# Performance work log

Hardware: AMD Instinct MI355X
Metric: run time of the kernel (lower is better)

The kernel has to match this reference:

```python
import jax, jax.numpy as jnp
import numpy as np

NUM_NEIGHBORS = (10, 25)  # FLAGS.num_neighbors = '10_25'
MAX_DEGREE = 64
L = 2  # num encoder layers


def _sample(nodes, neighbors_out, neighbors_in, key):
    """Multi-hop uniform neighbor sampling (shuffle columns + slice, as in TF code)."""
    samples = [nodes]
    support = 1
    supports = [1]
    for k in range(L):
        t = L - 1 - k
        n = NUM_NEIGHBORS[t]
        support *= 2 * n
        supports.append(support)
        key, k1, k2 = jax.random.split(key, 3)
        # tf.transpose(tf.random.shuffle(tf.transpose(x))) shuffles neighbor slots
        # with ONE permutation shared across all rows, then slices first n.
        cols_out = jax.random.permutation(k1, MAX_DEGREE)[:n]
        cols_in = jax.random.permutation(k2, MAX_DEGREE)[:n]
        nout = neighbors_out[samples[k]][:, cols_out]  # [prev, n]
        nin = neighbors_in[samples[k]][:, cols_in]     # [prev, n]
        samples.append(jnp.concatenate([nout, nin], axis=1).reshape(-1))
    return samples, supports


def _gc(self_v, nei_out, nei_in, W):
    # GraphConvolution: mean-aggregate out/in neighbors, concat with self, linear, sigmoid.
    agg = jnp.concatenate([self_v, nei_out.mean(axis=1), nei_in.mean(axis=1)], axis=-1)
    return jax.nn.sigmoid(agg @ W)


def _aggregate(inputs, supports, layer, W, B):
    h_hop = []
    for hop in range(L - layer):
        n = NUM_NEIGHBORS[L - hop - 1]
        nei = inputs[hop + 1].reshape(B * supports[hop], 2 * n, -1)
        self_v = inputs[hop].reshape(B * supports[hop], -1)
        h_hop.append(_gc(self_v, nei[:, :n], nei[:, n:], W))
    return h_hop


def _forward(nodes1, nodes2, neighbors_out, neighbors_in, features,
             W_in, W_mean, W_std, W_pi, W_ag, W_ad, Wd_mean, Wd_std, Wd_pi):
    B = nodes1.shape[0]
    key = jax.random.key(42)
    k1, k2 = jax.random.split(key)
    s1, sup1 = _sample(nodes1, neighbors_out, neighbors_in, k1)
    s2, sup2 = _sample(nodes2, neighbors_out, neighbors_in, k2)
    in1 = [features[s] for s in s1]  # hop-wise gathered features
    in2 = [features[s] for s in s2]
    # layer 0: shared input GC
    h1 = _aggregate(in1, sup1, 0, W_in, B)
    h2 = _aggregate(in2, sup2, 0, W_in, B)
    # layer 1: parameter heads (mean/std/pi/alpha)
    h_mean1 = _aggregate(h1, sup1, 1, W_mean, B)[0]
    h_mean2 = _aggregate(h2, sup2, 1, W_mean, B)[0]
    h_std1 = _aggregate(h1, sup1, 1, W_std, B)[0]
    h_std2 = _aggregate(h2, sup2, 1, W_std, B)[0]
    h_pi1 = _aggregate(h1, sup1, 1, W_pi, B)[0]
    h_pi2 = _aggregate(h2, sup2, 1, W_pi, B)[0]
    # final fully-connected projections (act = identity)
    z_mean1 = h_mean1 @ Wd_mean
    z_mean2 = h_mean2 @ Wd_mean
    z_std1 = h_std1 @ Wd_std
    z_std2 = h_std2 @ Wd_std
    pi_logit1 = h_pi1 @ Wd_pi
    pi_logit2 = h_pi2 @ Wd_pi
    return jnp.stack([z_mean1, z_std1, pi_logit1, z_mean2, z_std2, pi_logit2])


def setup_inputs() -> dict:
    key = jax.random.key(0)
    ks = jax.random.split(key, 16)
    N, F, B = 200000, 128, 256
    E, D = 128, 64
    inp = {
        'nodes1': jax.random.randint(ks[0], (B,), 0, N, dtype=jnp.int32),
        'nodes2': jax.random.randint(ks[1], (B,), 0, N, dtype=jnp.int32),
        'neighbors_out': jax.random.randint(ks[2], (N, MAX_DEGREE), 0, N, dtype=jnp.int32),
        'neighbors_in': jax.random.randint(ks[3], (N, MAX_DEGREE), 0, N, dtype=jnp.int32),
        'features': jax.random.normal(ks[4], (N, F), dtype=jnp.float32),
        'W_in': jax.random.normal(ks[5], (3 * F, E), dtype=jnp.float32) * 0.05,
        'W_mean': jax.random.normal(ks[6], (3 * E, E), dtype=jnp.float32) * 0.05,
        'W_std': jax.random.normal(ks[7], (3 * E, E), dtype=jnp.float32) * 0.05,
        'W_pi': jax.random.normal(ks[8], (3 * E, E), dtype=jnp.float32) * 0.05,
        'W_ag': jax.random.normal(ks[9], (3 * E, E), dtype=jnp.float32) * 0.05,
        'W_ad': jax.random.normal(ks[10], (3 * E, E), dtype=jnp.float32) * 0.05,
        'Wd_mean': jax.random.normal(ks[11], (E, D), dtype=jnp.float32) * 0.05,
        'Wd_std': jax.random.normal(ks[12], (E, D), dtype=jnp.float32) * 0.05,
        'Wd_pi': jax.random.normal(ks[13], (E, D), dtype=jnp.float32) * 0.05,
    }
    return inp


def reference(nodes1, nodes2, neighbors_out, neighbors_in, features,
              W_in, W_mean, W_std, W_pi, W_ag, W_ad, Wd_mean, Wd_std, Wd_pi):
    return _forward(nodes1, nodes2, neighbors_out, neighbors_in, features,
                    W_in, W_mean, W_std, W_pi, W_ag, W_ad, Wd_mean, Wd_std, Wd_pi)
```

## Files before the change

kernel.cpp:

```cpp
#include <hip/hip_runtime.h>
#include <stdint.h>
#include <math.h>

#define FDIM 128
#define KDIM 384
#define NROWS 26112

struct Cols { int o25[25]; int i25[25]; int o10[10]; int i10[10]; };
struct ColsBoth { Cols c[2]; };

static inline uint32_t rotl32(uint32_t x, uint32_t r){ return (x<<r)|(x>>(32u-r)); }

static void tf2x32(uint32_t k0, uint32_t k1, uint32_t c0, uint32_t c1,
                   uint32_t& o0, uint32_t& o1){
  const uint32_t ra[4] = {13u,15u,26u,6u};
  const uint32_t rb[4] = {17u,29u,16u,24u};
  uint32_t ks2 = k0 ^ k1 ^ 0x1BD11BDAu;
  uint32_t x0 = c0 + k0, x1 = c1 + k1;
  for(int i=0;i<4;i++){ x0 += x1; x1 = rotl32(x1, ra[i]); x1 ^= x0; }
  x0 += k1; x1 += ks2 + 1u;
  for(int i=0;i<4;i++){ x0 += x1; x1 = rotl32(x1, rb[i]); x1 ^= x0; }
  x0 += ks2; x1 += k0 + 2u;
  for(int i=0;i<4;i++){ x0 += x1; x1 = rotl32(x1, ra[i]); x1 ^= x0; }
  x0 += k0; x1 += k1 + 3u;
  for(int i=0;i<4;i++){ x0 += x1; x1 = rotl32(x1, rb[i]); x1 ^= x0; }
  x0 += k1; x1 += ks2 + 4u;
  for(int i=0;i<4;i++){ x0 += x1; x1 = rotl32(x1, ra[i]); x1 ^= x0; }
  x0 += ks2; x1 += k0 + 5u;
  o0 = x0; o1 = x1;
}

static void jax_split_child(uint32_t ka, uint32_t kb, uint32_t i,
                            uint32_t& oa, uint32_t& ob){
  tf2x32(ka, kb, 0u, i, oa, ob);
}

static uint32_t jax_bits32(uint32_t ka, uint32_t kb, uint32_t i){
  uint32_t a,b; tf2x32(ka, kb, 0u, i, a, b);
  return a ^ b;
}

static void jax_perm64(uint32_t ka, uint32_t kb, int* perm){
  uint32_t sa, sb; jax_split_child(ka, kb, 1u, sa, sb);
  uint32_t b[64]; int v[64];
  for(int i=0;i<64;i++){ b[i]=jax_bits32(sa, sb, (uint32_t)i); v[i]=i; }
  for(int i=1;i<64;i++){
    uint32_t bb=b[i]; int vv=v[i]; int j=i-1;
    while(j>=0 && b[j]>bb){ b[j+1]=b[j]; v[j+1]=v[j]; j--; }
    b[j+1]=bb; v[j+1]=vv;
  }
  for(int i=0;i<64;i++) perm[i]=v[i];
}

static void compute_cols(ColsBoth& cb){
  uint32_t k1a,k1b,k2a,k2b;
  jax_split_child(0u, 42u, 0u, k1a, k1b);
  jax_split_child(0u, 42u, 1u, k2a, k2b);
  for(int side=0; side<2; side++){
    uint32_t ka = side ? k2a : k1a;
    uint32_t kb = side ? k2b : k1b;
    uint32_t nka,nkb, c1a,c1b, c2a,c2b;
    jax_split_child(ka,kb,0u,nka,nkb);
    jax_split_child(ka,kb,1u,c1a,c1b);
    jax_split_child(ka,kb,2u,c2a,c2b);
    int p[64];
    jax_perm64(c1a,c1b,p); for(int i=0;i<25;i++) cb.c[side].o25[i]=p[i];
    jax_perm64(c2a,c2b,p); for(int i=0;i<25;i++) cb.c[side].i25[i]=p[i];
    uint32_t d1a,d1b,d2a,d2b;
    jax_split_child(nka,nkb,1u,d1a,d1b);
    jax_split_child(nka,nkb,2u,d2a,d2b);
    jax_perm64(d1a,d1b,p); for(int i=0;i<10;i++) cb.c[side].o10[i]=p[i];
    jax_perm64(d2a,d2b,p); for(int i=0;i<10;i++) cb.c[side].i10[i]=p[i];
  }
}

__device__ __forceinline__ float getc(const float4& v, int i){
  return (i==0)?v.x:(i==1)?v.y:(i==2)?v.z:v.w;
}
__device__ __forceinline__ float sigf(float x){ return 1.0f/(1.0f+expf(-x)); }
__device__ __forceinline__ void add4(float4& s, const float4& v){
  s.x+=v.x; s.y+=v.y; s.z+=v.z; s.w+=v.w;
}


__global__ __launch_bounds__(256) void sample1_kernel(
    const int* __restrict__ nodes1, const int* __restrict__ nodes2,
    const int* __restrict__ nout, const int* __restrict__ nin,
    int* __restrict__ s_hop1, ColsBoth cb){
  int idx = blockIdx.x*blockDim.x + threadIdx.x;
  if(idx >= 2*256*50) return;
  int side = idx / (256*50);
  int rem  = idx % (256*50);
  int b = rem / 50, j = rem % 50;
  int node = (side ? nodes2 : nodes1)[b];
  const Cols& c = cb.c[side];
  int nbr = (j < 25) ? nout[(long)node*64 + c.o25[j]]
                     : nin [(long)node*64 + c.i25[j-25]];
  s_hop1[idx] = nbr;
}

__global__ __launch_bounds__(256) void gather_kernel(
    const float* __restrict__ feat,
    const int* __restrict__ nodes1, const int* __restrict__ nodes2,
    const int* __restrict__ s_hop1,
    const int* __restrict__ nout, const int* __restrict__ nin,
    float* __restrict__ agg, int base_row, ColsBoth cb)
{
  int t = threadIdx.x;
  int row_local = blockIdx.x*8 + (t>>5);
  int lane = t & 31;
  int c0 = lane*4;
  int row = base_row + row_local;

  float4 selfv, so, si;

  if(row < 512){
    int side = row >> 8, b = row & 255;
    int node = (side ? nodes2 : nodes1)[b];
    selfv = *(const float4*)(feat + (long)node*FDIM + c0);
    const int* nb = s_hop1 + row*50;
    float4 acc = make_float4(0,0,0,0);
    #pragma unroll
    for(int jj=0; jj<25; jj+=5){
      int id[5]; float4 v[5];
      #pragma unroll
      for(int i=0;i<5;i++) id[i] = nb[jj+i];
      #pragma unroll
      for(int i=0;i<5;i++) v[i] = *(const float4*)(feat + (long)id[i]*FDIM + c0);
      #pragma unroll
      for(int i=0;i<5;i++) add4(acc, v[i]);
    }
    so = make_float4(acc.x/25.f, acc.y/25.f, acc.z/25.f, acc.w/25.f);
    acc = make_float4(0,0,0,0);
    #pragma unroll
    for(int jj=25; jj<50; jj+=5){
      int id[5]; float4 v[5];
      #pragma unroll
      for(int i=0;i<5;i++) id[i] = nb[jj+i];
      #pragma unroll
      for(int i=0;i<5;i++) v[i] = *(const float4*)(feat + (long)id[i]*FDIM + c0);
      #pragma unroll
      for(int i=0;i<5;i++) add4(acc, v[i]);
    }
    si = make_float4(acc.x/25.f, acc.y/25.f, acc.z/25.f, acc.w/25.f);
  } else {
    int hrow = row - 512;
    int side = (hrow >= 12800) ? 1 : 0;
    int node = s_hop1[hrow];
    const Cols& c = cb.c[side];
    const long nb = (long)node*64;
    int oid[10], iid[10];
    #pragma unroll
    for(int j=0;j<10;j++) oid[j] = nout[nb + c.o10[j]];
    #pragma unroll
    for(int j=0;j<10;j++) iid[j] = nin[nb + c.i10[j]];
    selfv = *(const float4*)(feat + (long)node*FDIM + c0);
    float4 v[10];
    #pragma unroll
    for(int j=0;j<10;j++) v[j] = *(const float4*)(feat + (long)oid[j]*FDIM + c0);
    float4 acc = make_float4(0,0,0,0);
    #pragma unroll
    for(int j=0;j<10;j++) add4(acc, v[j]);
    so = make_float4(acc.x*0.1f, acc.y*0.1f, acc.z*0.1f, acc.w*0.1f);
    #pragma unroll
    for(int j=0;j<10;j++) v[j] = *(const float4*)(feat + (long)iid[j]*FDIM + c0);
    acc = make_float4(0,0,0,0);
    #pragma unroll
    for(int j=0;j<10;j++) add4(acc, v[j]);
    si = make_float4(acc.x*0.1f, acc.y*0.1f, acc.z*0.1f, acc.w*0.1f);
  }

  float* ar = agg + (long)row_local*KDIM;
  *(float4*)(ar + c0)       = selfv;
  *(float4*)(ar + 128 + c0) = so;
  *(float4*)(ar + 256 + c0) = si;
}

__global__ __launch_bounds__(256) void gemm_sig_kernel(
    const float* __restrict__ A, const float* __restrict__ W,
    float* __restrict__ out)
{
  __shared__ float Wbuf[96*128];
  int t = threadIdx.x, lane = t&15, rg = t>>4;
  int r0 = blockIdx.x*64 + rg*4;
  int c0 = lane*8;
  float acc[4][8];
  #pragma unroll
  for(int r=0;r<4;r++)
    #pragma unroll
    for(int i=0;i<8;i++) acc[r][i]=0.f;

  for(int kc=0; kc<4; kc++){
    __syncthreads();
    const float4* ws = (const float4*)(W + kc*96*128);
    float4* wd = (float4*)Wbuf;
    #pragma unroll
    for(int i=0;i<12;i++) wd[i*256+t] = ws[i*256+t];
    __syncthreads();
    const float* Ab = A + (long)r0*KDIM + kc*96;
    #pragma unroll 2
    for(int k4=0;k4<96;k4+=4){
      float4 a0 = *(const float4*)(Ab + 0*KDIM + k4);
      float4 a1 = *(const float4*)(Ab + 1*KDIM + k4);
      float4 a2 = *(const float4*)(Ab + 2*KDIM + k4);
      float4 a3 = *(const float4*)(Ab + 3*KDIM + k4);
      #pragma unroll
      for(int kk=0;kk<4;kk++){
        float av0=getc(a0,kk), av1=getc(a1,kk), av2=getc(a2,kk), av3=getc(a3,kk);
        const float* wr = Wbuf + (k4+kk)*128 + c0;
        float4 w0 = *(const float4*)wr;
        float4 w1 = *(const float4*)(wr+4);
        acc[0][0]+=av0*w0.x; acc[0][1]+=av0*w0.y; acc[0][2]+=av0*w0.z; acc[0][3]+=av0*w0.w;
        acc[0][4]+=av0*w1.x; acc[0][5]+=av0*w1.y; acc[0][6]+=av0*w1.z; acc[0][7]+=av0*w1.w;
        acc[1][0]+=av1*w0.x; acc[1][1]+=av1*w0.y; acc[1][2]+=av1*w0.z; acc[1][3]+=av1*w0.w;
        acc[1][4]+=av1*w1.x; acc[1][5]+=av1*w1.y; acc[1][6]+=av1*w1.z; acc[1][7]+=av1*w1.w;
        acc[2][0]+=av2*w0.x; acc[2][1]+=av2*w0.y; acc[2][2]+=av2*w0.z; acc[2][3]+=av2*w0.w;
        acc[2][4]+=av2*w1.x; acc[2][5]+=av2*w1.y; acc[2][6]+=av2*w1.z; acc[2][7]+=av2*w1.w;
        acc[3][0]+=av3*w0.x; acc[3][1]+=av3*w0.y; acc[3][2]+=av3*w0.z; acc[3][3]+=av3*w0.w;
        acc[3][4]+=av3*w1.x; acc[3][5]+=av3*w1.y; acc[3][6]+=av3*w1.z; acc[3][7]+=av3*w1.w;
      }
    }
  }
  #pragma unroll
  for(int r=0;r<4;r++){
    float4 o0, o1;
    o0.x=sigf(acc[r][0]); o0.y=sigf(acc[r][1]); o0.z=sigf(acc[r][2]); o0.w=sigf(acc[r][3]);
    o1.x=sigf(acc[r][4]); o1.y=sigf(acc[r][5]); o1.z=sigf(acc[r][6]); o1.w=sigf(acc[r][7]);
    float* op = out + (long)(r0+r)*FDIM + c0;
    *(float4*)op = o0; *(float4*)(op+4) = o1;
  }
}

__global__ __launch_bounds__(256) void agg1_kernel(
    const float* __restrict__ h0, const float* __restrict__ h1,
    float* __restrict__ agg2)
{
  int row = blockIdx.x;
  int t = threadIdx.x;
  int ch = t & 127;
  int half = t >> 7;
  const float* base = h1 + (long)row*50*FDIM + half*25*FDIM + ch;
  float s = 0.f;
  #pragma unroll
  for(int j=0;j<25;j++) s += base[j*FDIM];
  agg2[(long)row*KDIM + 128 + half*128 + ch] = s * (1.0f/25.0f);
  if(half == 0) agg2[(long)row*KDIM + ch] = h0[(long)row*FDIM + ch];
}

__global__ __launch_bounds__(256) void head_kernel(
    const float* __restrict__ agg2,
    const float* __restrict__ Wm, const float* __restrict__ Ws, const float* __restrict__ Wp,
    const float* __restrict__ Dm, const float* __restrict__ Ds, const float* __restrict__ Dp,
    float* __restrict__ out)
{
  __shared__ float Wbuf[96*128];
  __shared__ float hb[64*133];
  int t = threadIdx.x, lane = t&15, rg = t>>4;
  int head = blockIdx.x >> 3, tile = blockIdx.x & 7;
  int r0t = tile*64;
  int r0 = r0t + rg*4;
  int c0 = lane*8;
  const float* W = (head==0) ? Wm : (head==1) ? Ws : Wp;
  const float* D = (head==0) ? Dm : (head==1) ? Ds : Dp;

  float acc[4][8];
  #pragma unroll
  for(int r=0;r<4;r++)
    #pragma unroll
    for(int i=0;i<8;i++) acc[r][i]=0.f;

  for(int kc=0; kc<4; kc++){
    __syncthreads();
    const float4* ws = (const float4*)(W + kc*96*128);
    float4* wd = (float4*)Wbuf;
    #pragma unroll
    for(int i=0;i<12;i++) wd[i*256+t] = ws[i*256+t];
    __syncthreads();
    const float* Ab = agg2 + (long)r0*KDIM + kc*96;
    #pragma unroll 2
    for(int k4=0;k4<96;k4+=4){
      float4 a0 = *(const float4*)(Ab + 0*KDIM + k4);
      float4 a1 = *(const float4*)(Ab + 1*KDIM + k4);
      float4 a2 = *(const float4*)(Ab + 2*KDIM + k4);
      float4 a3 = *(const float4*)(Ab + 3*KDIM + k4);
      #pragma unroll
      for(int kk=0;kk<4;kk++){
        float av0=getc(a0,kk), av1=getc(a1,kk), av2=getc(a2,kk), av3=getc(a3,kk);
        const float* wr = Wbuf + (k4+kk)*128 + c0;
        float4 w0 = *(const float4*)wr;
        float4 w1 = *(const float4*)(wr+4);
        acc[0][0]+=av0*w0.x; acc[0][1]+=av0*w0.y; acc[0][2]+=av0*w0.z; acc[0][3]+=av0*w0.w;
        acc[0][4]+=av0*w1.x; acc[0][5]+=av0*w1.y; acc[0][6]+=av0*w1.z; acc[0][7]+=av0*w1.w;
        acc[1][0]+=av1*w0.x; acc[1][1]+=av1*w0.y; acc[1][2]+=av1*w0.z; acc[1][3]+=av1*w0.w;
        acc[1][4]+=av1*w1.x; acc[1][5]+=av1*w1.y; acc[1][6]+=av1*w1.z; acc[1][7]+=av1*w1.w;
        acc[2][0]+=av2*w0.x; acc[2][1]+=av2*w0.y; acc[2][2]+=av2*w0.z; acc[2][3]+=av2*w0.w;
        acc[2][4]+=av2*w1.x; acc[2][5]+=av2*w1.y; acc[2][6]+=av2*w1.z; acc[2][7]+=av2*w1.w;
        acc[3][0]+=av3*w0.x; acc[3][1]+=av3*w0.y; acc[3][2]+=av3*w0.z; acc[3][3]+=av3*w0.w;
        acc[3][4]+=av3*w1.x; acc[3][5]+=av3*w1.y; acc[3][6]+=av3*w1.z; acc[3][7]+=av3*w1.w;
      }
    }
  }
  #pragma unroll
  for(int r=0;r<4;r++){
    float* hp = hb + (rg*4+r)*133 + c0;
    #pragma unroll
    for(int i=0;i<8;i++) hp[i] = sigf(acc[r][i]);
  }
  __syncthreads();
  {
    const float4* ds = (const float4*)D;
    float4* dd = (float4*)Wbuf;
    #pragma unroll
    for(int i=0;i<8;i++) dd[i*256+t] = ds[i*256+t];
  }
  __syncthreads();
  {
    int cd = lane*4;
    float a2[4][4];
    #pragma unroll
    for(int r=0;r<4;r++)
      #pragma unroll
      for(int i=0;i<4;i++) a2[r][i]=0.f;
    #pragma unroll 4
    for(int k=0;k<FDIM;k++){
      float4 d = *(const float4*)(Wbuf + k*64 + cd);
      #pragma unroll
      for(int r=0;r<4;r++){
        float hv = hb[(rg*4+r)*133 + k];
        a2[r][0]+=hv*d.x; a2[r][1]+=hv*d.y; a2[r][2]+=hv*d.z; a2[r][3]+=hv*d.w;
      }
    }
    #pragma unroll
    for(int r=0;r<4;r++){
      int row = r0 + r;
      int side = row >> 8, b = row & 255;
      float* op = out + ((long)(side*3+head)*256 + b)*64 + cd;
      *(float4*)op = make_float4(a2[r][0],a2[r][1],a2[r][2],a2[r][3]);
    }
  }
}

extern "C" void kernel_launch(void* const* d_in, const int* in_sizes, int n_in,
                              void* d_out, int out_size, void* d_ws, size_t ws_size,
                              hipStream_t stream) {
  const int*   nodes1  = (const int*)d_in[0];
  const int*   nodes2  = (const int*)d_in[1];
  const int*   nout    = (const int*)d_in[2];
  const int*   nin     = (const int*)d_in[3];
  const float* feat    = (const float*)d_in[4];
  const float* W_in    = (const float*)d_in[5];
  const float* W_mean  = (const float*)d_in[6];
  const float* W_std   = (const float*)d_in[7];
  const float* W_pi    = (const float*)d_in[8];
  const float* Wd_mean = (const float*)d_in[11];
  const float* Wd_std  = (const float*)d_in[12];
  const float* Wd_pi   = (const float*)d_in[13];
  float* out = (float*)d_out;

  int*   s_hop1 = (int*)d_ws;
  float* h      = (float*)(s_hop1 + 25600);
  float* agg2   = h + (size_t)NROWS*FDIM;
  float* aggC   = agg2 + 512*KDIM;

  size_t fixedB = 25600*4 + (size_t)NROWS*FDIM*4 + 512*KDIM*4;
  const int ncOpt[5] = {1,2,4,8,24};
  int nc = 24;
  for(int i=0;i<5;i++){
    size_t need = fixedB + ((size_t)NROWS/ncOpt[i])*KDIM*4;
    if(need <= ws_size){ nc = ncOpt[i]; break; }
  }
  int chunkRows = NROWS / nc;

  ColsBoth cb;
  compute_cols(cb);

  sample1_kernel<<<(2*256*50 + 255)/256, 256, 0, stream>>>(nodes1, nodes2, nout, nin, s_hop1, cb);
  for(int c=0;c<nc;c++){
    int base = c*chunkRows;
    gather_kernel<<<chunkRows/8, 256, 0, stream>>>(feat, nodes1, nodes2, s_hop1,
                                                   nout, nin, aggC, base, cb);
    gemm_sig_kernel<<<chunkRows/64, 256, 0, stream>>>(aggC, W_in, h + (size_t)base*FDIM);
  }
  agg1_kernel<<<512, 256, 0, stream>>>(h, h + 512*FDIM, agg2);
  head_kernel<<<24, 256, 0, stream>>>(agg2, W_mean, W_std, W_pi, Wd_mean, Wd_std, Wd_pi, out);
}
```

Baseline: 333.6 us.

## Fuse hop-1 aggregation into head kernel, enlarge GEMM row tile, batch gathers

Merges the agg1 and head kernels into one agghead kernel. It builds the 384-wide aggregated rows in shared memory and runs the head GEMM and the decoder straight from global weights over 96 blocks of 16 rows each, which removes the agg2 round trip and one launch. The main layer-0 GEMM now computes 8 rows per thread (128-row tiles), which raises register use but halves the number of shared-memory weight reads per FMA. The gather kernel now issues all 20 hop-1 neighbor loads before reducing, and the chunk-count options change so they divide evenly into 128-row tiles.

Measured after the change: 355.7 us. 6.6% more time.

```diff
diff --git a/kernel.cpp b/kernel.cpp
--- a/kernel.cpp
+++ b/kernel.cpp
@@ -155,18 +155,18 @@
     #pragma unroll
     for(int j=0;j<10;j++) iid[j] = nin[nb + c.i10[j]];
     selfv = *(const float4*)(feat + (long)node*FDIM + c0);
-    float4 v[10];
-    #pragma unroll
-    for(int j=0;j<10;j++) v[j] = *(const float4*)(feat + (long)oid[j]*FDIM + c0);
+    float4 v[20];
+    #pragma unroll
+    for(int j=0;j<10;j++) v[j]    = *(const float4*)(feat + (long)oid[j]*FDIM + c0);
+    #pragma unroll
+    for(int j=0;j<10;j++) v[10+j] = *(const float4*)(feat + (long)iid[j]*FDIM + c0);
     float4 acc = make_float4(0,0,0,0);
     #pragma unroll
     for(int j=0;j<10;j++) add4(acc, v[j]);
     so = make_float4(acc.x*0.1f, acc.y*0.1f, acc.z*0.1f, acc.w*0.1f);
-    #pragma unroll
-    for(int j=0;j<10;j++) v[j] = *(const float4*)(feat + (long)iid[j]*FDIM + c0);
     acc = make_float4(0,0,0,0);
     #pragma unroll
-    for(int j=0;j<10;j++) add4(acc, v[j]);
+    for(int j=0;j<10;j++) add4(acc, v[10+j]);
     si = make_float4(acc.x*0.1f, acc.y*0.1f, acc.z*0.1f, acc.w*0.1f);
   }
 
@@ -182,11 +182,11 @@
 {
   __shared__ float Wbuf[96*128];
   int t = threadIdx.x, lane = t&15, rg = t>>4;
-  int r0 = blockIdx.x*64 + rg*4;
+  int r0 = blockIdx.x*128 + rg*8;
   int c0 = lane*8;
-  float acc[4][8];
+  float acc[8][8];
   #pragma unroll
-  for(int r=0;r<4;r++)
+  for(int r=0;r<8;r++)
     #pragma unroll
     for(int i=0;i<8;i++) acc[r][i]=0.f;
 
@@ -198,31 +198,26 @@
     for(int i=0;i<12;i++) wd[i*256+t] = ws[i*256+t];
     __syncthreads();
     const float* Ab = A + (long)r0*KDIM + kc*96;
-    #pragma unroll 2
     for(int k4=0;k4<96;k4+=4){
-      float4 a0 = *(const float4*)(Ab + 0*KDIM + k4);
-      float4 a1 = *(const float4*)(Ab + 1*KDIM + k4);
-      float4 a2 = *(const float4*)(Ab + 2*KDIM + k4);
-      float4 a3 = *(const float4*)(Ab + 3*KDIM + k4);
+      float4 a[8];
+      #pragma unroll
+      for(int r=0;r<8;r++) a[r] = *(const float4*)(Ab + r*KDIM + k4);
       #pragma unroll
       for(int kk=0;kk<4;kk++){
-        float av0=getc(a0,kk), av1=getc(a1,kk), av2=getc(a2,kk), av3=getc(a3,kk);
         const float* wr = Wbuf + (k4+kk)*128 + c0;
         float4 w0 = *(const float4*)wr;
         float4 w1 = *(const float4*)(wr+4);
-        acc[0][0]+=av0*w0.x; acc[0][1]+=av0*w0.y; acc[0][2]+=av0*w0.z; acc[0][3]+=av0*w0.w;
-        acc[0][4]+=av0*w1.x; acc[0][5]+=av0*w1.y; acc[0][6]+=av0*w1.z; acc[0][7]+=av0*w1.w;
-        acc[1][0]+=av1*w0.x; acc[1][1]+=av1*w0.y; acc[1][2]+=av1*w0.z; acc[1][3]+=av1*w0.w;
-        acc[1][4]+=av1*w1.x; acc[1][5]+=av1*w1.y; acc[1][6]+=av1*w1.z; acc[1][7]+=av1*w1.w;
-        acc[2][0]+=av2*w0.x; acc[2][1]+=av2*w0.y; acc[2][2]+=av2*w0.z; acc[2][3]+=av2*w0.w;
-        acc[2][4]+=av2*w1.x; acc[2][5]+=av2*w1.y; acc[2][6]+=av2*w1.z; acc[2][7]+=av2*w1.w;
-        acc[3][0]+=av3*w0.x; acc[3][1]+=av3*w0.y; acc[3][2]+=av3*w0.z; acc[3][3]+=av3*w0.w;
-        acc[3][4]+=av3*w1.x; acc[3][5]+=av3*w1.y; acc[3][6]+=av3*w1.z; acc[3][7]+=av3*w1.w;
+        #pragma unroll
+        for(int r=0;r<8;r++){
+          float av = getc(a[r],kk);
+          acc[r][0]+=av*w0.x; acc[r][1]+=av*w0.y; acc[r][2]+=av*w0.z; acc[r][3]+=av*w0.w;
+          acc[r][4]+=av*w1.x; acc[r][5]+=av*w1.y; acc[r][6]+=av*w1.z; acc[r][7]+=av*w1.w;
+        }
       }
     }
   }
   #pragma unroll
-  for(int r=0;r<4;r++){
+  for(int r=0;r<8;r++){
     float4 o0, o1;
     o0.x=sigf(acc[r][0]); o0.y=sigf(acc[r][1]); o0.z=sigf(acc[r][2]); o0.w=sigf(acc[r][3]);
     o1.x=sigf(acc[r][4]); o1.y=sigf(acc[r][5]); o1.z=sigf(acc[r][6]); o1.w=sigf(acc[r][7]);
@@ -231,112 +226,86 @@
   }
 }
 
-__global__ __launch_bounds__(256) void agg1_kernel(
-    const float* __restrict__ h0, const float* __restrict__ h1,
-    float* __restrict__ agg2)
-{
-  int row = blockIdx.x;
-  int t = threadIdx.x;
-  int ch = t & 127;
-  int half = t >> 7;
-  const float* base = h1 + (long)row*50*FDIM + half*25*FDIM + ch;
-  float s = 0.f;
-  #pragma unroll
-  for(int j=0;j<25;j++) s += base[j*FDIM];
-  agg2[(long)row*KDIM + 128 + half*128 + ch] = s * (1.0f/25.0f);
-  if(half == 0) agg2[(long)row*KDIM + ch] = h0[(long)row*FDIM + ch];
-}
-
-__global__ __launch_bounds__(256) void head_kernel(
-    const float* __restrict__ agg2,
+__global__ __launch_bounds__(256) void agghead_kernel(
+    const float* __restrict__ h,
     const float* __restrict__ Wm, const float* __restrict__ Ws, const float* __restrict__ Wp,
     const float* __restrict__ Dm, const float* __restrict__ Ds, const float* __restrict__ Dp,
     float* __restrict__ out)
 {
-  __shared__ float Wbuf[96*128];
-  __shared__ float hb[64*133];
+  __shared__ float agg[16][388];
+  __shared__ float hb[16][132];
+  int head = blockIdx.x >> 5, tile = blockIdx.x & 31;
   int t = threadIdx.x, lane = t&15, rg = t>>4;
-  int head = blockIdx.x >> 3, tile = blockIdx.x & 7;
-  int r0t = tile*64;
-  int r0 = r0t + rg*4;
+  int row = tile*16 + rg;
   int c0 = lane*8;
   const float* W = (head==0) ? Wm : (head==1) ? Ws : Wp;
   const float* D = (head==0) ? Dm : (head==1) ? Ds : Dp;
 
-  float acc[4][8];
-  #pragma unroll
-  for(int r=0;r<4;r++)
-    #pragma unroll
-    for(int i=0;i<8;i++) acc[r][i]=0.f;
-
-  for(int kc=0; kc<4; kc++){
-    __syncthreads();
-    const float4* ws = (const float4*)(W + kc*96*128);
-    float4* wd = (float4*)Wbuf;
-    #pragma unroll
-    for(int i=0;i<12;i++) wd[i*256+t] = ws[i*256+t];
-    __syncthreads();
-    const float* Ab = agg2 + (long)r0*KDIM + kc*96;
-    #pragma unroll 2
-    for(int k4=0;k4<96;k4+=4){
-      float4 a0 = *(const float4*)(Ab + 0*KDIM + k4);
-      float4 a1 = *(const float4*)(Ab + 1*KDIM + k4);
-      float4 a2 = *(const float4*)(Ab + 2*KDIM + k4);
-      float4 a3 = *(const float4*)(Ab + 3*KDIM + k4);
-      #pragma unroll
-      for(int kk=0;kk<4;kk++){
-        float av0=getc(a0,kk), av1=getc(a1,kk), av2=getc(a2,kk), av3=getc(a3,kk);
-        const float* wr = Wbuf + (k4+kk)*128 + c0;
-        float4 w0 = *(const float4*)wr;
-        float4 w1 = *(const float4*)(wr+4);
-        acc[0][0]+=av0*w0.x; acc[0][1]+=av0*w0.y; acc[0][2]+=av0*w0.z; acc[0][3]+=av0*w0.w;
-        acc[0][4]+=av0*w1.x; acc[0][5]+=av0*w1.y; acc[0][6]+=av0*w1.z; acc[0][7]+=av0*w1.w;
-        acc[1][0]+=av1*w0.x; acc[1][1]+=av1*w0.y; acc[1][2]+=av1*w0.z; acc[1][3]+=av1*w0.w;
-        acc[1][4]+=av1*w1.x; acc[1][5]+=av1*w1.y; acc[1][6]+=av1*w1.z; acc[1][7]+=av1*w1.w;
-        acc[2][0]+=av2*w0.x; acc[2][1]+=av2*w0.y; acc[2][2]+=av2*w0.z; acc[2][3]+=av2*w0.w;
-        acc[2][4]+=av2*w1.x; acc[2][5]+=av2*w1.y; acc[2][6]+=av2*w1.z; acc[2][7]+=av2*w1.w;
-        acc[3][0]+=av3*w0.x; acc[3][1]+=av3*w0.y; acc[3][2]+=av3*w0.z; acc[3][3]+=av3*w0.w;
-        acc[3][4]+=av3*w1.x; acc[3][5]+=av3*w1.y; acc[3][6]+=av3*w1.z; acc[3][7]+=av3*w1.w;
+  {
+    const float* sp = h + (long)row*FDIM + c0;
+    *(float4*)&agg[rg][c0]   = *(const float4*)sp;
+    *(float4*)&agg[rg][c0+4] = *(const float4*)(sp+4);
+    const float* base = h + (long)(512 + row*50)*FDIM + c0;
+    float4 s0 = make_float4(0,0,0,0), s1 = make_float4(0,0,0,0);
+    #pragma unroll
+    for(int jj=0;jj<25;jj+=5){
+      float4 v0[5], v1[5];
+      #pragma unroll
+      for(int i=0;i<5;i++){
+        const float* fp = base + (long)(jj+i)*FDIM;
+        v0[i] = *(const float4*)fp; v1[i] = *(const float4*)(fp+4);
       }
-    }
-  }
-  #pragma unroll
-  for(int r=0;r<4;r++){
-    float* hp = hb + (rg*4+r)*133 + c0;
-    #pragma unroll
-    for(int i=0;i<8;i++) hp[i] = sigf(acc[r][i]);
+      #pragma unroll
+      for(int i=0;i<5;i++){ add4(s0, v0[i]); add4(s1, v1[i]); }
+    }
+    const float inv = 1.0f/25.0f;
+    *(float4*)&agg[rg][128+c0]   = make_float4(s0.x*inv,s0.y*inv,s0.z*inv,s0.w*inv);
+    *(float4*)&agg[rg][128+c0+4] = make_float4(s1.x*inv,s1.y*inv,s1.z*inv,s1.w*inv);
+    s0 = make_float4(0,0,0,0); s1 = make_float4(0,0,0,0);
+    #pragma unroll
+    for(int jj=25;jj<50;jj+=5){
+      float4 v0[5], v1[5];
+      #pragma unroll
+      for(int i=0;i<5;i++){
+        const float* fp = base + (long)(jj+i)*FDIM;
+        v0[i] = *(const float4*)fp; v1[i] = *(const float4*)(fp+4);
+      }
+      #pragma unroll
+      for(int i=0;i<5;i++){ add4(s0, v0[i]); add4(s1, v1[i]); }
+    }
+    *(float4*)&agg[rg][256+c0]   = make_float4(s0.x*inv,s0.y*inv,s0.z*inv,s0.w*inv);
+    *(float4*)&agg[rg][256+c0+4] = make_float4(s1.x*inv,s1.y*inv,s1.z*inv,s1.w*inv);
   }
   __syncthreads();
+
   {
-    const float4* ds = (const float4*)D;
-    float4* dd = (float4*)Wbuf;
-    #pragma unroll
-    for(int i=0;i<8;i++) dd[i*256+t] = ds[i*256+t];
+    float acc[8] = {0,0,0,0,0,0,0,0};
+    #pragma unroll 4
+    for(int k=0;k<KDIM;k++){
+      float a = agg[rg][k];
+      const float* wr = W + (long)k*FDIM + c0;
+      float4 w0 = *(const float4*)wr; float4 w1 = *(const float4*)(wr+4);
+      acc[0]+=a*w0.x; acc[1]+=a*w0.y; acc[2]+=a*w0.z; acc[3]+=a*w0.w;
+      acc[4]+=a*w1.x; acc[5]+=a*w1.y; acc[6]+=a*w1.z; acc[7]+=a*w1.w;
+    }
+    #pragma unroll
+    for(int i=0;i<8;i++) hb[rg][c0+i] = sigf(acc[i]);
   }
   __syncthreads();
+
   {
     int cd = lane*4;
-    float a2[4][4];
-    #pragma unroll
-    for(int r=0;r<4;r++)
-      #pragma unroll
-      for(int i=0;i<4;i++) a2[r][i]=0.f;
+    float a0=0,a1=0,a2=0,a3=0;
     #pragma unroll 4
     for(int k=0;k<FDIM;k++){
-      float4 d = *(const float4*)(Wbuf + k*64 + cd);
-      #pragma unroll
-      for(int r=0;r<4;r++){
-        float hv = hb[(rg*4+r)*133 + k];
-        a2[r][0]+=hv*d.x; a2[r][1]+=hv*d.y; a2[r][2]+=hv*d.z; a2[r][3]+=hv*d.w;
-      }
-    }
-    #pragma unroll
-    for(int r=0;r<4;r++){
-      int row = r0 + r;
-      int side = row >> 8, b = row & 255;
-      float* op = out + ((long)(side*3+head)*256 + b)*64 + cd;
-      *(float4*)op = make_float4(a2[r][0],a2[r][1],a2[r][2],a2[r][3]);
-    }
+      float hv = hb[rg][k];
+      const float* dr = D + (long)k*64 + cd;
+      float4 d = *(const float4*)dr;
+      a0 += hv*d.x; a1 += hv*d.y; a2 += hv*d.z; a3 += hv*d.w;
+    }
+    int side = row >> 8, b = row & 255;
+    float* op = out + ((long)(side*3+head)*256 + b)*64 + cd;
+    *(float4*)op = make_float4(a0,a1,a2,a3);
   }
 }
 
@@ -359,12 +328,11 @@
 
   int*   s_hop1 = (int*)d_ws;
   float* h      = (float*)(s_hop1 + 25600);
-  float* agg2   = h + (size_t)NROWS*FDIM;
-  float* aggC   = agg2 + 512*KDIM;
-
-  size_t fixedB = 25600*4 + (size_t)NROWS*FDIM*4 + 512*KDIM*4;
-  const int ncOpt[5] = {1,2,4,8,24};
-  int nc = 24;
+  float* aggC   = h + (size_t)NROWS*FDIM;
+
+  size_t fixedB = 25600*4 + (size_t)NROWS*FDIM*4;
+  const int ncOpt[5] = {1,2,4,12,51};
+  int nc = 51;
   for(int i=0;i<5;i++){
     size_t need = fixedB + ((size_t)NROWS/ncOpt[i])*KDIM*4;
     if(need <= ws_size){ nc = ncOpt[i]; break; }
@@ -379,8 +347,7 @@
     int base = c*chunkRows;
     gather_kernel<<<chunkRows/8, 256, 0, stream>>>(feat, nodes1, nodes2, s_hop1,
                                                    nout, nin, aggC, base, cb);
-    gemm_sig_kernel<<<chunkRows/64, 256, 0, stream>>>(aggC, W_in, h + (size_t)base*FDIM);
-  }
-  agg1_kernel<<<512, 256, 0, stream>>>(h, h + 512*FDIM, agg2);
-  head_kernel<<<24, 256, 0, stream>>>(agg2, W_mean, W_std, W_pi, Wd_mean, Wd_std, Wd_pi, out);
-}
+    gemm_sig_kernel<<<chunkRows/128, 256, 0, stream>>>(aggC, W_in, h + (size_t)base*FDIM);
+  }
+  agghead_kernel<<<96, 256, 0, stream>>>(h, W_mean, W_std, W_pi, Wd_mean, Wd_std, Wd_pi, out);
+}
```

## Spread head kernel across many small blocks, batch hop-1 gather loads

Applied to the files above, without the earlier changes.

The head kernel now gives each block 4 rows, so 384 blocks run instead of 24. Weights are read directly from global memory or cache instead of being staged and tiled in shared memory, which trades register tiling for parallelism across the GPU. The gather kernel issues all 20 neighbour loads before reducing, for more memory-level parallelism. The fallback chunk counts change so chunkRows stays a multiple of 64.

Result: no change. 331.1 us (-0.8%).

```diff
diff --git a/kernel.cpp b/kernel.cpp
--- a/kernel.cpp
+++ b/kernel.cpp
@@ -155,18 +155,18 @@
     #pragma unroll
     for(int j=0;j<10;j++) iid[j] = nin[nb + c.i10[j]];
     selfv = *(const float4*)(feat + (long)node*FDIM + c0);
-    float4 v[10];
-    #pragma unroll
-    for(int j=0;j<10;j++) v[j] = *(const float4*)(feat + (long)oid[j]*FDIM + c0);
+    float4 v[20];
+    #pragma unroll
+    for(int j=0;j<10;j++) v[j]    = *(const float4*)(feat + (long)oid[j]*FDIM + c0);
+    #pragma unroll
+    for(int j=0;j<10;j++) v[10+j] = *(const float4*)(feat + (long)iid[j]*FDIM + c0);
     float4 acc = make_float4(0,0,0,0);
     #pragma unroll
     for(int j=0;j<10;j++) add4(acc, v[j]);
     so = make_float4(acc.x*0.1f, acc.y*0.1f, acc.z*0.1f, acc.w*0.1f);
-    #pragma unroll
-    for(int j=0;j<10;j++) v[j] = *(const float4*)(feat + (long)iid[j]*FDIM + c0);
     acc = make_float4(0,0,0,0);
     #pragma unroll
-    for(int j=0;j<10;j++) add4(acc, v[j]);
+    for(int j=0;j<10;j++) add4(acc, v[10+j]);
     si = make_float4(acc.x*0.1f, acc.y*0.1f, acc.z*0.1f, acc.w*0.1f);
   }
 
@@ -253,90 +253,46 @@
     const float* __restrict__ Dm, const float* __restrict__ Ds, const float* __restrict__ Dp,
     float* __restrict__ out)
 {
-  __shared__ float Wbuf[96*128];
-  __shared__ float hb[64*133];
-  int t = threadIdx.x, lane = t&15, rg = t>>4;
-  int head = blockIdx.x >> 3, tile = blockIdx.x & 7;
-  int r0t = tile*64;
-  int r0 = r0t + rg*4;
-  int c0 = lane*8;
+  __shared__ float As[4*KDIM];
+  __shared__ float Hs[4*FDIM];
+  int head = blockIdx.x >> 7;
+  int rt   = blockIdx.x & 127;
+  int t = threadIdx.x;
+  int row = t >> 6;
+  int c = (t & 63) * 2;
   const float* W = (head==0) ? Wm : (head==1) ? Ws : Wp;
   const float* D = (head==0) ? Dm : (head==1) ? Ds : Dp;
 
-  float acc[4][8];
-  #pragma unroll
-  for(int r=0;r<4;r++)
-    #pragma unroll
-    for(int i=0;i<8;i++) acc[r][i]=0.f;
-
-  for(int kc=0; kc<4; kc++){
-    __syncthreads();
-    const float4* ws = (const float4*)(W + kc*96*128);
-    float4* wd = (float4*)Wbuf;
-    #pragma unroll
-    for(int i=0;i<12;i++) wd[i*256+t] = ws[i*256+t];
-    __syncthreads();
-    const float* Ab = agg2 + (long)r0*KDIM + kc*96;
-    #pragma unroll 2
-    for(int k4=0;k4<96;k4+=4){
-      float4 a0 = *(const float4*)(Ab + 0*KDIM + k4);
-      float4 a1 = *(const float4*)(Ab + 1*KDIM + k4);
-      float4 a2 = *(const float4*)(Ab + 2*KDIM + k4);
-      float4 a3 = *(const float4*)(Ab + 3*KDIM + k4);
-      #pragma unroll
-      for(int kk=0;kk<4;kk++){
-        float av0=getc(a0,kk), av1=getc(a1,kk), av2=getc(a2,kk), av3=getc(a3,kk);
-        const float* wr = Wbuf + (k4+kk)*128 + c0;
-        float4 w0 = *(const float4*)wr;
-        float4 w1 = *(const float4*)(wr+4);
-        acc[0][0]+=av0*w0.x; acc[0][1]+=av0*w0.y; acc[0][2]+=av0*w0.z; acc[0][3]+=av0*w0.w;
-        acc[0][4]+=av0*w1.x; acc[0][5]+=av0*w1.y; acc[0][6]+=av0*w1.z; acc[0][7]+=av0*w1.w;
-        acc[1][0]+=av1*w0.x; acc[1][1]+=av1*w0.y; acc[1][2]+=av1*w0.z; acc[1][3]+=av1*w0.w;
-        acc[1][4]+=av1*w1.x; acc[1][5]+=av1*w1.y; acc[1][6]+=av1*w1.z; acc[1][7]+=av1*w1.w;
-        acc[2][0]+=av2*w0.x; acc[2][1]+=av2*w0.y; acc[2][2]+=av2*w0.z; acc[2][3]+=av2*w0.w;
-        acc[2][4]+=av2*w1.x; acc[2][5]+=av2*w1.y; acc[2][6]+=av2*w1.z; acc[2][7]+=av2*w1.w;
-        acc[3][0]+=av3*w0.x; acc[3][1]+=av3*w0.y; acc[3][2]+=av3*w0.z; acc[3][3]+=av3*w0.w;
-        acc[3][4]+=av3*w1.x; acc[3][5]+=av3*w1.y; acc[3][6]+=av3*w1.z; acc[3][7]+=av3*w1.w;
-      }
+  {
+    const float* src = agg2 + (long)rt*4*KDIM;
+    #pragma unroll
+    for(int i=0;i<6;i++) As[i*256 + t] = src[i*256 + t];
+  }
+  __syncthreads();
+
+  float acc0 = 0.f, acc1 = 0.f;
+  const float* as = As + row*KDIM;
+  #pragma unroll 8
+  for(int k=0;k<KDIM;k++){
+    float a = as[k];
+    float2 w = *(const float2*)(W + (long)k*FDIM + c);
+    acc0 += a*w.x; acc1 += a*w.y;
+  }
+  Hs[row*FDIM + c]   = sigf(acc0);
+  Hs[row*FDIM + c+1] = sigf(acc1);
+  __syncthreads();
+
+  {
+    int col = t & 63;
+    const float* hs = Hs + row*FDIM;
+    float a = 0.f;
+    #pragma unroll 8
+    for(int k=0;k<FDIM;k++){
+      a += hs[k] * D[(long)k*64 + col];
     }
-  }
-  #pragma unroll
-  for(int r=0;r<4;r++){
-    float* hp = hb + (rg*4+r)*133 + c0;
-    #pragma unroll
-    for(int i=0;i<8;i++) hp[i] = sigf(acc[r][i]);
-  }
-  __syncthreads();
-  {
-    const float4* ds = (const float4*)D;
-    float4* dd = (float4*)Wbuf;
-    #pragma unroll
-    for(int i=0;i<8;i++) dd[i*256+t] = ds[i*256+t];
-  }
-  __syncthreads();
-  {
-    int cd = lane*4;
-    float a2[4][4];
-    #pragma unroll
-    for(int r=0;r<4;r++)
-      #pragma unroll
-      for(int i=0;i<4;i++) a2[r][i]=0.f;
-    #pragma unroll 4
-    for(int k=0;k<FDIM;k++){
-      float4 d = *(const float4*)(Wbuf + k*64 + cd);
-      #pragma unroll
-      for(int r=0;r<4;r++){
-        float hv = hb[(rg*4+r)*133 + k];
-        a2[r][0]+=hv*d.x; a2[r][1]+=hv*d.y; a2[r][2]+=hv*d.z; a2[r][3]+=hv*d.w;
-      }
-    }
-    #pragma unroll
-    for(int r=0;r<4;r++){
-      int row = r0 + r;
-      int side = row >> 8, b = row & 255;
-      float* op = out + ((long)(side*3+head)*256 + b)*64 + cd;
-      *(float4*)op = make_float4(a2[r][0],a2[r][1],a2[r][2],a2[r][3]);
-    }
+    int grow = rt*4 + row;
+    int side = grow >> 8, b = grow & 255;
+    out[((long)(side*3+head)*256 + b)*64 + col] = a;
   }
 }
 
@@ -363,8 +319,8 @@
   float* aggC   = agg2 + 512*KDIM;
 
   size_t fixedB = 25600*4 + (size_t)NROWS*FDIM*4 + 512*KDIM*4;
-  const int ncOpt[5] = {1,2,4,8,24};
-  int nc = 24;
+  const int ncOpt[5] = {1,2,4,12,51};
+  int nc = 51;
   for(int i=0;i<5;i++){
     size_t need = fixedB + ((size_t)NROWS/ncOpt[i])*KDIM*4;
     if(need <= ws_size){ nc = ncOpt[i]; break; }
@@ -382,5 +338,5 @@
     gemm_sig_kernel<<<chunkRows/64, 256, 0, stream>>>(aggC, W_in, h + (size_t)base*FDIM);
   }
   agg1_kernel<<<512, 256, 0, stream>>>(h, h + 512*FDIM, agg2);
-  head_kernel<<<24, 256, 0, stream>>>(agg2, W_mean, W_std, W_pi, Wd_mean, Wd_std, Wd_pi, out);
-}
+  head_kernel<<<384, 256, 0, stream>>>(agg2, W_mean, W_std, W_pi, Wd_mean, Wd_std, Wd_pi, out);
+}
```
